# Kernel tuning notes

Measured on AMD Instinct MI355X. Metric: run time of the kernel, lower is better.

Reference implementation:

```python
import jax, jax.numpy as jnp
import numpy as np

EPS = 1e-12  # F.normalize default eps


def setup_inputs() -> dict:
    key = jax.random.key(0)
    x = jax.random.normal(key, (4, 64, 8192, 1), dtype=jnp.float32)
    return {"x": x, "k": 9, "dilation": 1}


def reference(x, k, dilation):
    # x: (B, D, N, 1)
    B, D, N, _ = x.shape
    kk = k * dilation
    # F.normalize(x, p=2, dim=1)
    norm = jnp.linalg.norm(x, axis=1, keepdims=True)
    xn = x / jnp.maximum(norm, EPS)
    # -> (B, N, D)
    pts = jnp.squeeze(xn, -1).transpose(0, 2, 1)
    # pairwise euclidean distance (cdist p=2)
    sq = jnp.sum(pts * pts, axis=-1)  # (B, N)
    d2 = sq[:, :, None] + sq[:, None, :] - 2.0 * jnp.einsum("bnd,bmd->bnm", pts, pts)
    dist = jnp.sqrt(jnp.maximum(d2, 0.0))  # (B, N, N)
    # torch.topk(-dist, k): k smallest distances
    _, nn_idx = jax.lax.top_k(-dist, kk)  # (B, N, kk)
    center_idx = jnp.broadcast_to(jnp.arange(N, dtype=nn_idx.dtype)[None, :, None], (B, N, kk))
    edge_index = jnp.stack([nn_idx, center_idx], axis=0)  # (2, B, N, kk)
    return edge_index[:, :, :, ::dilation]
```

## Files before the change

### kernel.cpp

```cpp
#include <hip/hip_runtime.h>

#define BB 4
#define DD 64
#define NN 8192
#define KK 9


typedef __attribute__((ext_vector_type(8))) _Float16 f16x8;
typedef __attribute__((ext_vector_type(16))) float f32x16;
typedef __attribute__((ext_vector_type(2))) _Float16 h2;
struct H2x4 { h2 a, b, c, d; };

__device__ __forceinline__ uint4 pack8(const unsigned* w) {
    return make_uint4(w[0] | (w[1] << 16), w[2] | (w[3] << 16),
                      w[4] | (w[5] << 16), w[6] | (w[7] << 16));
}

__device__ __forceinline__ float min3f(float a, float b, float c) {
    return fminf(fminf(a, b), c);
}

__device__ __forceinline__ float dot2acc(h2 g, h2 r, float acc) {
#if __has_builtin(__builtin_amdgcn_fdot2)
    return __builtin_amdgcn_fdot2(g, r, acc, false);
#else
    acc = fmaf((float)g[0], (float)r[0], acc);
    return fmaf((float)g[1], (float)r[1], acc);
#endif
}

__device__ __forceinline__ int s_to_j(int g, int s4) {
    int T = ((g >> 6) << 5) + (((g >> 5) & 1) << 4) + (g & 15);
    return T * 32 + ((s4 >> 2) << 3) + (((g >> 4) & 1) << 2) + (s4 & 3);
}

__global__ __launch_bounds__(256) void knorm2_kernel(const float* __restrict__ x,
                                                     float* __restrict__ xnT,
                                                     float* __restrict__ sq,
                                                     unsigned short* __restrict__ Phi,
                                                     unsigned short* __restrict__ Shi) {
    int t = blockIdx.x * 256 + threadIdx.x;
    int b = t >> 13;
    int n = t & (NN - 1);
    const float* xb = x + (size_t)b * DD * NN + n;
    float v[DD];
    float ss = 0.0f;
#pragma unroll
    for (int d = 0; d < DD; ++d) {
        v[d] = xb[(size_t)d * NN];
        ss = fmaf(v[d], v[d], ss);
    }
    float inv = 1.0f / fmaxf(sqrtf(ss), 1e-12f);
    float s2 = 0.0f;
#pragma unroll
    for (int d = 0; d < DD; ++d) {
        v[d] *= inv;
        s2 = fmaf(v[d], v[d], s2);
    }
    sq[t] = s2;
    float4* o4 = reinterpret_cast<float4*>(xnT + (size_t)t * DD);
#pragma unroll
    for (int d = 0; d < DD; d += 4) o4[d >> 2] = make_float4(v[d], v[d+1], v[d+2], v[d+3]);

    size_t base = (size_t)t * DD;
#pragma unroll
    for (int d0 = 0; d0 < DD; d0 += 8) {
        unsigned ph[8], sh[8];
#pragma unroll
        for (int e = 0; e < 8; ++e) {
            float f = v[d0 + e];
            _Float16 hp = (_Float16)f;
            _Float16 hs = (_Float16)(-2.0f * f);
            ph[e] = (unsigned)__builtin_bit_cast(unsigned short, hp);
            sh[e] = (unsigned)__builtin_bit_cast(unsigned short, hs);
        }
        *reinterpret_cast<uint4*>(Phi + base + d0) = pack8(ph);
        *reinterpret_cast<uint4*>(Shi + base + d0) = pack8(sh);
    }
}

__global__ __launch_bounds__(256, 4) void kmin_kernel(const unsigned short* __restrict__ Shi,
                                                      const unsigned short* __restrict__ Phi,
                                                      unsigned short* __restrict__ minbuf16) {
    __shared__ float stage[4][64][33];
    const int lane = threadIdx.x & 63;
    const int wave = threadIdx.x >> 6;
    const int l31 = lane & 31;
    const int half = lane >> 5;
    const int i0 = blockIdx.x * 256 + wave * 64;
    const int b = i0 >> 13;
    const int jloc0 = blockIdx.y * (NN / 8);

    f16x8 Bh0[4], Bh1[4];
    {
        const size_t ib0 = (size_t)(i0 + l31) * DD + half * 8;
        const size_t ib1 = (size_t)(i0 + 32 + l31) * DD + half * 8;
#pragma unroll
        for (int kc = 0; kc < 4; ++kc) {
            Bh0[kc] = *reinterpret_cast<const f16x8*>(Phi + ib0 + kc * 16);
            Bh1[kc] = *reinterpret_cast<const f16x8*>(Phi + ib1 + kc * 16);
        }
    }
    const size_t ja0 = ((size_t)b * NN + jloc0 + l31) * DD + half * 8;

    f16x8 A0[4], A1[4];
#pragma unroll
    for (int kc = 0; kc < 4; ++kc)
        A0[kc] = *reinterpret_cast<const f16x8*>(Shi + ja0 + kc * 16);

#pragma unroll 2
    for (int u2 = 0; u2 < 16; ++u2) {
        const int t0 = u2 * 2;
        {
            const size_t ja = ja0 + (size_t)(t0 + 1) * 32 * DD;
#pragma unroll
            for (int kc = 0; kc < 4; ++kc)
                A1[kc] = *reinterpret_cast<const f16x8*>(Shi + ja + kc * 16);
        }
        {
            f32x16 c0 = {}, c1 = {};
#pragma unroll
            for (int kc = 0; kc < 4; ++kc)
                c0 = __builtin_amdgcn_mfma_f32_32x32x16_f16(A0[kc], Bh0[kc], c0, 0, 0, 0);
#pragma unroll
            for (int kc = 0; kc < 4; ++kc)
                c1 = __builtin_amdgcn_mfma_f32_32x32x16_f16(A0[kc], Bh1[kc], c1, 0, 0, 0);
            const int col = half * 16 + (t0 & 15);
            {
                float q0 = min3f(c0[0], c0[1], c0[2]);
                float q1 = min3f(c0[3], c0[4], c0[5]);
                float q2 = min3f(c0[6], c0[7], c0[8]);
                float q3 = min3f(c0[9], c0[10], c0[11]);
                float q4 = min3f(c0[12], c0[13], c0[14]);
                stage[wave][l31][col] = fminf(min3f(q0, q1, q2), min3f(q3, q4, c0[15]));
            }
            {
                float q0 = min3f(c1[0], c1[1], c1[2]);
                float q1 = min3f(c1[3], c1[4], c1[5]);
                float q2 = min3f(c1[6], c1[7], c1[8]);
                float q3 = min3f(c1[9], c1[10], c1[11]);
                float q4 = min3f(c1[12], c1[13], c1[14]);
                stage[wave][32 + l31][col] = fminf(min3f(q0, q1, q2), min3f(q3, q4, c1[15]));
            }
        }
        if (u2 < 15) {
            const size_t ja = ja0 + (size_t)(t0 + 2) * 32 * DD;
#pragma unroll
            for (int kc = 0; kc < 4; ++kc)
                A0[kc] = *reinterpret_cast<const f16x8*>(Shi + ja + kc * 16);
        }
        {
            f32x16 c0 = {}, c1 = {};
#pragma unroll
            for (int kc = 0; kc < 4; ++kc)
                c0 = __builtin_amdgcn_mfma_f32_32x32x16_f16(A1[kc], Bh0[kc], c0, 0, 0, 0);
#pragma unroll
            for (int kc = 0; kc < 4; ++kc)
                c1 = __builtin_amdgcn_mfma_f32_32x32x16_f16(A1[kc], Bh1[kc], c1, 0, 0, 0);
            const int col = half * 16 + ((t0 + 1) & 15);
            {
                float q0 = min3f(c0[0], c0[1], c0[2]);
                float q1 = min3f(c0[3], c0[4], c0[5]);
                float q2 = min3f(c0[6], c0[7], c0[8]);
                float q3 = min3f(c0[9], c0[10], c0[11]);
                float q4 = min3f(c0[12], c0[13], c0[14]);
                stage[wave][l31][col] = fminf(min3f(q0, q1, q2), min3f(q3, q4, c0[15]));
            }
            {
                float q0 = min3f(c1[0], c1[1], c1[2]);
                float q1 = min3f(c1[3], c1[4], c1[5]);
                float q2 = min3f(c1[6], c1[7], c1[8]);
                float q3 = min3f(c1[9], c1[10], c1[11]);
                float q4 = min3f(c1[12], c1[13], c1[14]);
                stage[wave][32 + l31][col] = fminf(min3f(q0, q1, q2), min3f(q3, q4, c1[15]));
            }
        }
        if ((t0 & 15) == 14) {
            const int fph = t0 >> 4;
            unsigned short* dst0 = minbuf16 + (size_t)blockIdx.y * 64 + fph * 32;
#pragma unroll
            for (int it = 0; it < 4; ++it) {
                int idx = it * 64 + lane;
                int r = idx >> 2;
                int p = idx & 3;
                const float* s = &stage[wave][r][p * 8];
                unsigned w[8];
#pragma unroll
                for (int e = 0; e < 8; ++e)
                    w[e] = (unsigned)__builtin_bit_cast(unsigned short, (_Float16)s[e]);
                *reinterpret_cast<uint4*>(dst0 + (size_t)(i0 + r) * 512 + p * 8) = pack8(w);
            }
        }
    }
}

__global__ __launch_bounds__(256) void ksel_kernel(const float* __restrict__ xnT,
                                                   const float* __restrict__ sq,
                                                   const unsigned short* __restrict__ minbuf16,
                                                   const unsigned short* __restrict__ Phi,
                                                   int* __restrict__ out) {
    __shared__ unsigned short glist[4][40];
    __shared__ unsigned short jlist[4][64];
    const int lane = threadIdx.x & 63;
    const int wave = threadIdx.x >> 6;
    const int t = blockIdx.x * 4 + wave;
    const int tu = __builtin_amdgcn_readfirstlane(t);
    const int b = tu >> 13;
    const int n = tu & (NN - 1);

    float gm[8];
    {
        uint4 a = *reinterpret_cast<const uint4*>(minbuf16 + (size_t)tu * 512 + lane * 8);
        unsigned wv[4] = {a.x, a.y, a.z, a.w};
#pragma unroll
        for (int q4 = 0; q4 < 4; ++q4) {
            gm[q4 * 2 + 0] = (float)__builtin_bit_cast(_Float16, (unsigned short)(wv[q4] & 0xFFFFu));
            gm[q4 * 2 + 1] = (float)__builtin_bit_cast(_Float16, (unsigned short)(wv[q4] >> 16));
        }
    }

    float sv = fminf(min3f(gm[0], gm[1], gm[2]),
                     fminf(min3f(gm[3], gm[4], gm[5]), fminf(gm[6], gm[7])));
#pragma unroll
    for (int k = 2; k <= 64; k <<= 1) {
#pragma unroll
        for (int jj = k >> 1; jj >= 1; jj >>= 1) {
            float o = __shfl_xor(sv, jj);
            bool keepMin = (((lane & jj) == 0) == ((lane & k) == 0));
            sv = keepMin ? fminf(sv, o) : fmaxf(sv, o);
        }
    }
    const float th9p = __shfl(sv, 8);
    const float theta  = th9p + 8e-3f;
    const float kappa1 = th9p + 7.5e-3f;

    int cnt = 0;
    unsigned short* gl = &glist[wave][0];
#pragma unroll
    for (int q = 0; q < 8; ++q) {
        bool c = gm[q] <= theta;
        unsigned long long mask = __ballot(c);
        int pos = cnt + __popcll(mask & ((1ULL << lane) - 1ULL));
        if (c && pos < 40) gl[pos] = (unsigned short)(lane * 8 + q);
        cnt += (int)__popcll(mask);
    }
    __syncthreads();

    const unsigned short* __restrict__ Pb = Phi + ((size_t)b * NN) * DD;
    H2x4 arh[8];
    {
        const f16x8* pr = reinterpret_cast<const f16x8*>(Phi + (size_t)tu * DD);
#pragma unroll
        for (int c8 = 0; c8 < 8; ++c8) arh[c8] = __builtin_bit_cast(H2x4, pr[c8]);
    }

    const bool ovf = (cnt > 40);
    const int total = ovf ? NN : cnt * 16;
    const int nIt = (total + 63) >> 6;
    int S1 = 0;
    unsigned short* jl = &jlist[wave][0];
#pragma unroll 1
    for (int m = 0; m < nIt; ++m) {
        const int idx = m * 64 + lane;
        const bool act = idx < total;
        float m2ap = __uint_as_float(0x7f800000u);
        int j = 0;
        if (act) {
            j = ovf ? idx : s_to_j((int)gl[idx >> 4], idx & 15);
            const f16x8* p8 = reinterpret_cast<const f16x8*>(Pb + (size_t)j * DD);
            float a0 = 0.0f, a1 = 0.0f, a2 = 0.0f, a3 = 0.0f;
#pragma unroll
            for (int c8 = 0; c8 < 8; ++c8) {
                H2x4 g2 = __builtin_bit_cast(H2x4, p8[c8]);
                a0 = dot2acc(g2.a, arh[c8].a, a0);
                a1 = dot2acc(g2.b, arh[c8].b, a1);
                a2 = dot2acc(g2.c, arh[c8].c, a2);
                a3 = dot2acc(g2.d, arh[c8].d, a3);
            }
            m2ap = -2.0f * ((a0 + a1) + (a2 + a3));
        }
        bool pass = act && (m2ap <= kappa1);
        unsigned long long mask = __ballot(pass);
        int pos = S1 + __popcll(mask & ((1ULL << lane) - 1ULL));
        if (pass && pos < 64) jl[pos] = (unsigned short)j;
        S1 += (int)__popcll(mask);
    }
    __syncthreads();

    const float* __restrict__ Bb = xnT + (size_t)b * NN * DD;
    const float* __restrict__ sqb = sq + (size_t)b * NN;
    float ar[DD];
    {
        const float4* a4 = reinterpret_cast<const float4*>(xnT + (size_t)tu * DD);
#pragma unroll
        for (int d = 0; d < DD; d += 4) {
            float4 f = a4[d >> 2];
            ar[d] = f.x; ar[d + 1] = f.y; ar[d + 2] = f.z; ar[d + 3] = f.w;
        }
    }

    unsigned long long kout = ~0ULL;
    if (S1 <= 64) {
        unsigned long long v = ~0ULL;
        if (lane < S1) {
            int j = (int)jl[lane];
            const float4* bc4 = reinterpret_cast<const float4*>(Bb + (size_t)j * DD);
            float a0 = 0.0f, a1 = 0.0f, a2 = 0.0f, a3 = 0.0f;
#pragma unroll
            for (int d4 = 0; d4 < DD / 4; ++d4) {
                float4 f = bc4[d4];
                a0 = fmaf(ar[4 * d4 + 0], f.x, a0);
                a1 = fmaf(ar[4 * d4 + 1], f.y, a1);
                a2 = fmaf(ar[4 * d4 + 2], f.z, a2);
                a3 = fmaf(ar[4 * d4 + 3], f.w, a3);
            }
            float dot = (a0 + a1) + (a2 + a3);
            float key = fmaf(-2.0f, dot, sqb[j]);
            unsigned ub = __float_as_uint(key);
            ub ^= (0x80000000u | (unsigned)((int)ub >> 31));
            v = ((unsigned long long)ub << 32) | (unsigned)j;
        }
#pragma unroll
        for (int k = 2; k <= 64; k <<= 1) {
#pragma unroll
            for (int jj = k >> 1; jj >= 1; jj >>= 1) {
                unsigned long long o = __shfl_xor(v, jj);
                bool keepMin = (((lane & jj) == 0) == ((lane & k) == 0));
                bool less = o < v;
                unsigned long long mn = less ? o : v;
                unsigned long long mx = less ? v : o;
                v = keepMin ? mn : mx;
            }
        }
        kout = v;
    } else {
        unsigned long long kd[KK];
#pragma unroll
        for (int m = 0; m < KK; ++m) kd[m] = ~0ULL;
#pragma unroll 1
        for (int m = 0; m < nIt; ++m) {
            const int idx = m * 64 + lane;
            if (idx >= total) continue;
            int j = ovf ? idx : s_to_j((int)gl[idx >> 4], idx & 15);
            const float4* bc4 = reinterpret_cast<const float4*>(Bb + (size_t)j * DD);
            float a0 = 0.0f, a1 = 0.0f, a2 = 0.0f, a3 = 0.0f;
#pragma unroll
            for (int d4 = 0; d4 < DD / 4; ++d4) {
                float4 f = bc4[d4];
                a0 = fmaf(ar[4 * d4 + 0], f.x, a0);
                a1 = fmaf(ar[4 * d4 + 1], f.y, a1);
                a2 = fmaf(ar[4 * d4 + 2], f.z, a2);
                a3 = fmaf(ar[4 * d4 + 3], f.w, a3);
            }
            float dot = (a0 + a1) + (a2 + a3);
            float key = fmaf(-2.0f, dot, sqb[j]);
            unsigned ub = __float_as_uint(key);
            ub ^= (0x80000000u | (unsigned)((int)ub >> 31));
            unsigned long long cnd = ((unsigned long long)ub << 32) | (unsigned)j;
            if (cnd < kd[KK - 1]) {
#pragma unroll
                for (int m2 = 0; m2 < KK; ++m2) {
                    bool sw = cnd < kd[m2];
                    unsigned long long lo = sw ? cnd : kd[m2];
                    unsigned long long hi = sw ? kd[m2] : cnd;
                    kd[m2] = lo;
                    cnd = hi;
                }
            }
        }
#pragma unroll
        for (int r = 0; r < KK; ++r) {
            unsigned long long c = kd[0];
            unsigned long long wm = c;
#pragma unroll
            for (int d = 1; d < 64; d <<= 1) {
                unsigned long long o = __shfl_xor(wm, d);
                wm = (o < wm) ? o : wm;
            }
            if (lane == r) kout = wm;
            if (c == wm) {
#pragma unroll
                for (int m2 = 0; m2 < KK - 1; ++m2) kd[m2] = kd[m2 + 1];
                kd[KK - 1] = ~0ULL;
            }
        }
    }

    if (lane < KK) {
        out[(size_t)tu * KK + lane] = (int)(kout & 0xFFFFFFFFULL);
        out[(size_t)BB * NN * KK + (size_t)tu * KK + lane] = n;
    }
}

__global__ __launch_bounds__(256) void knorm_kernel(const float* __restrict__ x,
                                                    float* __restrict__ xnT,
                                                    float* __restrict__ sq) {
    int t = blockIdx.x * 256 + threadIdx.x;
    int b = t >> 13;
    int n = t & (NN - 1);
    const float* xb = x + (size_t)b * DD * NN + n;
    float v[DD];
    float ss = 0.0f;
#pragma unroll
    for (int d = 0; d < DD; ++d) {
        v[d] = xb[(size_t)d * NN];
        ss = fmaf(v[d], v[d], ss);
    }
    float norm = sqrtf(ss);
    float inv = 1.0f / fmaxf(norm, 1e-12f);
    float s2 = 0.0f;
#pragma unroll
    for (int d = 0; d < DD; ++d) {
        float xv = v[d] * inv;
        v[d] = xv;
        s2 = fmaf(xv, xv, s2);
    }
    float4* o4 = reinterpret_cast<float4*>(xnT + (size_t)t * DD);
#pragma unroll
    for (int d = 0; d < DD; d += 4) {
        o4[d >> 2] = make_float4(v[d], v[d + 1], v[d + 2], v[d + 3]);
    }
    sq[t] = s2;
}

template <int S>
__global__ __launch_bounds__(256, 2) void kdist_kernel(const float* __restrict__ xnT,
                                                       const float* __restrict__ sq,
                                                       unsigned long long* __restrict__ cand) {
    const int rb = blockIdx.x;
    const int b = rb >> 5;
    const int nbase = (rb & 31) * 256;
    const int n = nbase + threadIdx.x;
    const int s = blockIdx.y;
    const int jcount = NN / S;
    const int j0 = s * jcount;
    const int j1 = j0 + jcount;

    const float* __restrict__ Bb = xnT + ((size_t)b * NN) * DD;
    const float* __restrict__ sqb = sq + (size_t)b * NN;

    float ar[DD];
    {
        const float4* a4 = reinterpret_cast<const float4*>(Bb + (size_t)n * DD);
#pragma unroll
        for (int d = 0; d < DD; d += 4) {
            float4 f = a4[d >> 2];
            ar[d] = f.x; ar[d + 1] = f.y; ar[d + 2] = f.z; ar[d + 3] = f.w;
        }
    }
#pragma unroll
    for (int d = 0; d < DD; ++d) {
        asm volatile("" : "+v"(ar[d]));
    }

    unsigned long long kd[KK];
#pragma unroll
    for (int m = 0; m < KK; ++m) kd[m] = ~0ULL;

#pragma unroll 2
    for (int j = j0; j < j1; ++j) {
        const float4* bc4 = reinterpret_cast<const float4*>(Bb + (size_t)j * DD);
        float a0 = 0.0f, a1 = 0.0f, a2 = 0.0f, a3 = 0.0f;
#pragma unroll
        for (int d4 = 0; d4 < DD / 4; ++d4) {
            float4 f = bc4[d4];
            a0 = fmaf(ar[4 * d4 + 0], f.x, a0);
            a1 = fmaf(ar[4 * d4 + 1], f.y, a1);
            a2 = fmaf(ar[4 * d4 + 2], f.z, a2);
            a3 = fmaf(ar[4 * d4 + 3], f.w, a3);
        }
        float dot = (a0 + a1) + (a2 + a3);
        float key = fmaf(-2.0f, dot, sqb[j]);
        unsigned int ub = __float_as_uint(key);
        ub ^= (0x80000000u | (unsigned int)((int)ub >> 31));
        unsigned long long cnd = ((unsigned long long)ub << 32) | (unsigned int)j;
        if (cnd < kd[KK - 1]) {
#pragma unroll
            for (int m = 0; m < KK; ++m) {
                bool sw = cnd < kd[m];
                unsigned long long lo = sw ? cnd : kd[m];
                unsigned long long hi = sw ? kd[m] : cnd;
                kd[m] = lo;
                cnd = hi;
            }
        }
    }

    unsigned long long* outc = cand + ((size_t)(b * NN + n) * S + s) * KK;
#pragma unroll
    for (int m = 0; m < KK; ++m) outc[m] = kd[m];
}

template <int S>
__global__ __launch_bounds__(256) void kmerge_kernel(const unsigned long long* __restrict__ cand,
                                                     int* __restrict__ out) {
    int t = blockIdx.x * 256 + threadIdx.x;
    const unsigned long long* c = cand + (size_t)t * (S * KK);
    unsigned long long kd[KK];
#pragma unroll
    for (int m = 0; m < KK; ++m) kd[m] = ~0ULL;
#pragma unroll
    for (int q = 0; q < S * KK; ++q) {
        unsigned long long cnd = c[q];
        if (cnd < kd[KK - 1]) {
#pragma unroll
            for (int m = 0; m < KK; ++m) {
                bool sw = cnd < kd[m];
                unsigned long long lo = sw ? cnd : kd[m];
                unsigned long long hi = sw ? kd[m] : cnd;
                kd[m] = lo;
                cnd = hi;
            }
        }
    }
    int n = t & (NN - 1);
    int* out0 = out + (size_t)t * KK;
    int* out1 = out + (size_t)BB * NN * KK + (size_t)t * KK;
#pragma unroll
    for (int m = 0; m < KK; ++m) {
        out0[m] = (int)(kd[m] & 0xFFFFFFFFULL);
        out1[m] = n;
    }
}

extern "C" void kernel_launch(void* const* d_in, const int* in_sizes, int n_in,
                              void* d_out, int out_size, void* d_ws, size_t ws_size,
                              hipStream_t stream) {
    const float* x = (const float*)d_in[0];
    int* out = (int*)d_out;
    char* ws = (char*)d_ws;

    constexpr size_t XNT_B = (size_t)BB * NN * DD * 4;
    constexpr size_t SQ_B  = (size_t)BB * NN * 4;
    float* xnT = (float*)ws;
    float* sq  = (float*)(ws + XNT_B);

    constexpr size_t BF_B  = (size_t)BB * NN * DD * 2;
    constexpr size_t OFF_PHI = XNT_B + SQ_B;
    constexpr size_t OFF_PLO = OFF_PHI + BF_B;
    constexpr size_t OFF_SHI = OFF_PLO + BF_B;
    constexpr size_t OFF_SLO = OFF_SHI + BF_B;
    constexpr size_t OFF_MIN = OFF_SLO + BF_B;
    constexpr size_t MIN_B   = (size_t)512 * BB * NN * 4;
    constexpr size_t NEED_NEW = OFF_MIN + MIN_B;

    if (ws_size >= NEED_NEW) {
        unsigned short* Phi = (unsigned short*)(ws + OFF_PHI);
        unsigned short* Shi = (unsigned short*)(ws + OFF_SHI);
        unsigned short* minbuf16 = (unsigned short*)(ws + OFF_MIN);

        knorm2_kernel<<<dim3(BB * NN / 256), dim3(256), 0, stream>>>(x, xnT, sq, Phi, Shi);
        kmin_kernel<<<dim3(BB * NN / 256, 8), dim3(256), 0, stream>>>(Shi, Phi, minbuf16);
        ksel_kernel<<<dim3(BB * NN / 4), dim3(256), 0, stream>>>(xnT, sq, minbuf16, Phi, out);
        return;
    }

    unsigned long long* cand = (unsigned long long*)(ws + XNT_B + SQ_B);
    const size_t base = XNT_B + SQ_B;
    const size_t need8 = base + (size_t)BB * NN * 8 * KK * 8;

    knorm_kernel<<<dim3(BB * NN / 256), dim3(256), 0, stream>>>(x, xnT, sq);
    if (ws_size >= need8) {
        kdist_kernel<8><<<dim3(BB * NN / 256, 8), dim3(256), 0, stream>>>(xnT, sq, cand);
        kmerge_kernel<8><<<dim3(BB * NN / 256), dim3(256), 0, stream>>>(cand, out);
    } else {
        kdist_kernel<4><<<dim3(BB * NN / 256, 4), dim3(256), 0, stream>>>(xnT, sq, cand);
        kmerge_kernel<4><<<dim3(BB * NN / 256), dim3(256), 0, stream>>>(cand, out);
    }
}
```

Before: 245.6 us.

## Process two query points per wave in ksel kernel to raise ILP

Each wave in the selection kernel now handles two query points, interleaving their threshold sort, group listing, fp16 prefilter and exact distance/bitonic sort so independent memory loads and shuffles can overlap. The __syncthreads barriers are removed because shared lists are per-wave, and the first float4s of candidate rows are prefetched before loading the query vector. The grid is halved to match. This raises register pressure (two sets of query fragments and sort state), which may lower occupancy, and the loop runs to the longer of the two candidate counts.

Measured after the change: 243.2 us. No clear change (-1.0%).

```diff
diff --git a/kernel.cpp b/kernel.cpp
--- a/kernel.cpp
+++ b/kernel.cpp
@@ -199,158 +199,260 @@
                                                    const unsigned short* __restrict__ minbuf16,
                                                    const unsigned short* __restrict__ Phi,
                                                    int* __restrict__ out) {
-    __shared__ unsigned short glist[4][40];
-    __shared__ unsigned short jlist[4][64];
+    __shared__ unsigned short glist[4][2][40];
+    __shared__ unsigned short jlist[4][2][64];
     const int lane = threadIdx.x & 63;
     const int wave = threadIdx.x >> 6;
-    const int t = blockIdx.x * 4 + wave;
-    const int tu = __builtin_amdgcn_readfirstlane(t);
-    const int b = tu >> 13;
-    const int n = tu & (NN - 1);
-
-    float gm[8];
+    const int tA = __builtin_amdgcn_readfirstlane(blockIdx.x * 8 + wave * 2);
+    const int tB = tA + 1;
+    const int b = tA >> 13;
+    const int nA = tA & (NN - 1);
+    const int nB = tB & (NN - 1);
+
+    float gmA[8], gmB[8];
     {
-        uint4 a = *reinterpret_cast<const uint4*>(minbuf16 + (size_t)tu * 512 + lane * 8);
-        unsigned wv[4] = {a.x, a.y, a.z, a.w};
+        uint4 a = *reinterpret_cast<const uint4*>(minbuf16 + (size_t)tA * 512 + lane * 8);
+        uint4 c = *reinterpret_cast<const uint4*>(minbuf16 + (size_t)tB * 512 + lane * 8);
+        unsigned wa[4] = {a.x, a.y, a.z, a.w};
+        unsigned wb[4] = {c.x, c.y, c.z, c.w};
 #pragma unroll
         for (int q4 = 0; q4 < 4; ++q4) {
-            gm[q4 * 2 + 0] = (float)__builtin_bit_cast(_Float16, (unsigned short)(wv[q4] & 0xFFFFu));
-            gm[q4 * 2 + 1] = (float)__builtin_bit_cast(_Float16, (unsigned short)(wv[q4] >> 16));
-        }
-    }
-
-    float sv = fminf(min3f(gm[0], gm[1], gm[2]),
-                     fminf(min3f(gm[3], gm[4], gm[5]), fminf(gm[6], gm[7])));
+            gmA[q4*2+0] = (float)__builtin_bit_cast(_Float16, (unsigned short)(wa[q4] & 0xFFFFu));
+            gmA[q4*2+1] = (float)__builtin_bit_cast(_Float16, (unsigned short)(wa[q4] >> 16));
+            gmB[q4*2+0] = (float)__builtin_bit_cast(_Float16, (unsigned short)(wb[q4] & 0xFFFFu));
+            gmB[q4*2+1] = (float)__builtin_bit_cast(_Float16, (unsigned short)(wb[q4] >> 16));
+        }
+    }
+
+    float svA = fminf(min3f(gmA[0], gmA[1], gmA[2]),
+                      fminf(min3f(gmA[3], gmA[4], gmA[5]), fminf(gmA[6], gmA[7])));
+    float svB = fminf(min3f(gmB[0], gmB[1], gmB[2]),
+                      fminf(min3f(gmB[3], gmB[4], gmB[5]), fminf(gmB[6], gmB[7])));
 #pragma unroll
     for (int k = 2; k <= 64; k <<= 1) {
 #pragma unroll
         for (int jj = k >> 1; jj >= 1; jj >>= 1) {
-            float o = __shfl_xor(sv, jj);
+            float oA = __shfl_xor(svA, jj);
+            float oB = __shfl_xor(svB, jj);
             bool keepMin = (((lane & jj) == 0) == ((lane & k) == 0));
-            sv = keepMin ? fminf(sv, o) : fmaxf(sv, o);
-        }
-    }
-    const float th9p = __shfl(sv, 8);
-    const float theta  = th9p + 8e-3f;
-    const float kappa1 = th9p + 7.5e-3f;
-
-    int cnt = 0;
-    unsigned short* gl = &glist[wave][0];
+            svA = keepMin ? fminf(svA, oA) : fmaxf(svA, oA);
+            svB = keepMin ? fminf(svB, oB) : fmaxf(svB, oB);
+        }
+    }
+    const float th9pA = __shfl(svA, 8);
+    const float th9pB = __shfl(svB, 8);
+    const float thetaA  = th9pA + 8e-3f,  thetaB  = th9pB + 8e-3f;
+    const float kappa1A = th9pA + 7.5e-3f, kappa1B = th9pB + 7.5e-3f;
+
+    int cntA = 0, cntB = 0;
+    unsigned short* glA = &glist[wave][0][0];
+    unsigned short* glB = &glist[wave][1][0];
 #pragma unroll
     for (int q = 0; q < 8; ++q) {
-        bool c = gm[q] <= theta;
-        unsigned long long mask = __ballot(c);
-        int pos = cnt + __popcll(mask & ((1ULL << lane) - 1ULL));
-        if (c && pos < 40) gl[pos] = (unsigned short)(lane * 8 + q);
-        cnt += (int)__popcll(mask);
-    }
-    __syncthreads();
+        bool cA = gmA[q] <= thetaA;
+        unsigned long long mA = __ballot(cA);
+        int pA = cntA + __popcll(mA & ((1ULL << lane) - 1ULL));
+        if (cA && pA < 40) glA[pA] = (unsigned short)(lane * 8 + q);
+        cntA += (int)__popcll(mA);
+        bool cB = gmB[q] <= thetaB;
+        unsigned long long mB = __ballot(cB);
+        int pB = cntB + __popcll(mB & ((1ULL << lane) - 1ULL));
+        if (cB && pB < 40) glB[pB] = (unsigned short)(lane * 8 + q);
+        cntB += (int)__popcll(mB);
+    }
 
     const unsigned short* __restrict__ Pb = Phi + ((size_t)b * NN) * DD;
-    H2x4 arh[8];
+    H2x4 arhA[8], arhB[8];
     {
-        const f16x8* pr = reinterpret_cast<const f16x8*>(Phi + (size_t)tu * DD);
-#pragma unroll
-        for (int c8 = 0; c8 < 8; ++c8) arh[c8] = __builtin_bit_cast(H2x4, pr[c8]);
-    }
-
-    const bool ovf = (cnt > 40);
-    const int total = ovf ? NN : cnt * 16;
-    const int nIt = (total + 63) >> 6;
-    int S1 = 0;
-    unsigned short* jl = &jlist[wave][0];
+        const f16x8* prA = reinterpret_cast<const f16x8*>(Phi + (size_t)tA * DD);
+        const f16x8* prB = reinterpret_cast<const f16x8*>(Phi + (size_t)tB * DD);
+#pragma unroll
+        for (int c8 = 0; c8 < 8; ++c8) {
+            arhA[c8] = __builtin_bit_cast(H2x4, prA[c8]);
+            arhB[c8] = __builtin_bit_cast(H2x4, prB[c8]);
+        }
+    }
+
+    const bool ovfA = (cntA > 40), ovfB = (cntB > 40);
+    const int totalA = ovfA ? NN : cntA * 16;
+    const int totalB = ovfB ? NN : cntB * 16;
+    const int nItA = (totalA + 63) >> 6, nItB = (totalB + 63) >> 6;
+    const int nIt = nItA > nItB ? nItA : nItB;
+    int S1A = 0, S1B = 0;
+    unsigned short* jlA = &jlist[wave][0][0];
+    unsigned short* jlB = &jlist[wave][1][0];
 #pragma unroll 1
     for (int m = 0; m < nIt; ++m) {
         const int idx = m * 64 + lane;
-        const bool act = idx < total;
-        float m2ap = __uint_as_float(0x7f800000u);
-        int j = 0;
-        if (act) {
-            j = ovf ? idx : s_to_j((int)gl[idx >> 4], idx & 15);
-            const f16x8* p8 = reinterpret_cast<const f16x8*>(Pb + (size_t)j * DD);
+        const bool actA = idx < totalA;
+        const bool actB = idx < totalB;
+        float m2A = __uint_as_float(0x7f800000u);
+        float m2B = __uint_as_float(0x7f800000u);
+        int jA = 0, jB = 0;
+        if (actA) {
+            jA = ovfA ? idx : s_to_j((int)glA[idx >> 4], idx & 15);
+            const f16x8* p8 = reinterpret_cast<const f16x8*>(Pb + (size_t)jA * DD);
             float a0 = 0.0f, a1 = 0.0f, a2 = 0.0f, a3 = 0.0f;
 #pragma unroll
             for (int c8 = 0; c8 < 8; ++c8) {
                 H2x4 g2 = __builtin_bit_cast(H2x4, p8[c8]);
-                a0 = dot2acc(g2.a, arh[c8].a, a0);
-                a1 = dot2acc(g2.b, arh[c8].b, a1);
-                a2 = dot2acc(g2.c, arh[c8].c, a2);
-                a3 = dot2acc(g2.d, arh[c8].d, a3);
-            }
-            m2ap = -2.0f * ((a0 + a1) + (a2 + a3));
-        }
-        bool pass = act && (m2ap <= kappa1);
-        unsigned long long mask = __ballot(pass);
-        int pos = S1 + __popcll(mask & ((1ULL << lane) - 1ULL));
-        if (pass && pos < 64) jl[pos] = (unsigned short)j;
-        S1 += (int)__popcll(mask);
-    }
-    __syncthreads();
+                a0 = dot2acc(g2.a, arhA[c8].a, a0);
+                a1 = dot2acc(g2.b, arhA[c8].b, a1);
+                a2 = dot2acc(g2.c, arhA[c8].c, a2);
+                a3 = dot2acc(g2.d, arhA[c8].d, a3);
+            }
+            m2A = -2.0f * ((a0 + a1) + (a2 + a3));
+        }
+        if (actB) {
+            jB = ovfB ? idx : s_to_j((int)glB[idx >> 4], idx & 15);
+            const f16x8* p8 = reinterpret_cast<const f16x8*>(Pb + (size_t)jB * DD);
+            float a0 = 0.0f, a1 = 0.0f, a2 = 0.0f, a3 = 0.0f;
+#pragma unroll
+            for (int c8 = 0; c8 < 8; ++c8) {
+                H2x4 g2 = __builtin_bit_cast(H2x4, p8[c8]);
+                a0 = dot2acc(g2.a, arhB[c8].a, a0);
+                a1 = dot2acc(g2.b, arhB[c8].b, a1);
+                a2 = dot2acc(g2.c, arhB[c8].c, a2);
+                a3 = dot2acc(g2.d, arhB[c8].d, a3);
+            }
+            m2B = -2.0f * ((a0 + a1) + (a2 + a3));
+        }
+        bool passA = actA && (m2A <= kappa1A);
+        unsigned long long mA = __ballot(passA);
+        int pA = S1A + __popcll(mA & ((1ULL << lane) - 1ULL));
+        if (passA && pA < 64) jlA[pA] = (unsigned short)jA;
+        S1A += (int)__popcll(mA);
+        bool passB = actB && (m2B <= kappa1B);
+        unsigned long long mB = __ballot(passB);
+        int pB = S1B + __popcll(mB & ((1ULL << lane) - 1ULL));
+        if (passB && pB < 64) jlB[pB] = (unsigned short)jB;
+        S1B += (int)__popcll(mB);
+    }
 
     const float* __restrict__ Bb = xnT + (size_t)b * NN * DD;
     const float* __restrict__ sqb = sq + (size_t)b * NN;
-    float ar[DD];
+
+    unsigned long long vA = ~0ULL, vB = ~0ULL;
     {
-        const float4* a4 = reinterpret_cast<const float4*>(xnT + (size_t)tu * DD);
+        float4 bufA[4], bufB[4];
+        int jA = 0, jB = 0;
+        const bool hvA = lane < (S1A <= 64 ? S1A : 64);
+        const bool hvB = lane < (S1B <= 64 ? S1B : 64);
+        if (hvA) {
+            jA = (int)jlA[lane];
+            const float4* bc4 = reinterpret_cast<const float4*>(Bb + (size_t)jA * DD);
+#pragma unroll
+            for (int p = 0; p < 4; ++p) bufA[p] = bc4[p * 4];
+        }
+        if (hvB) {
+            jB = (int)jlB[lane];
+            const float4* bc4 = reinterpret_cast<const float4*>(Bb + (size_t)jB * DD);
+#pragma unroll
+            for (int p = 0; p < 4; ++p) bufB[p] = bc4[p * 4];
+        }
+        {
+            float ar[DD];
+            const float4* a4 = reinterpret_cast<const float4*>(xnT + (size_t)tA * DD);
+#pragma unroll
+            for (int d = 0; d < DD; d += 4) {
+                float4 f = a4[d >> 2];
+                ar[d] = f.x; ar[d+1] = f.y; ar[d+2] = f.z; ar[d+3] = f.w;
+            }
+            if (hvA) {
+                const float4* bc4 = reinterpret_cast<const float4*>(Bb + (size_t)jA * DD);
+                float a0 = 0, a1 = 0, a2 = 0, a3 = 0;
+#pragma unroll
+                for (int d4 = 0; d4 < 16; ++d4) {
+                    float4 f = (d4 % 4 == 0) ? bufA[d4 / 4] : bc4[d4];
+                    a0 = fmaf(ar[4*d4+0], f.x, a0);
+                    a1 = fmaf(ar[4*d4+1], f.y, a1);
+                    a2 = fmaf(ar[4*d4+2], f.z, a2);
+                    a3 = fmaf(ar[4*d4+3], f.w, a3);
+                }
+                float dot = (a0 + a1) + (a2 + a3);
+                float key = fmaf(-2.0f, dot, sqb[jA]);
+                unsigned ub = __float_as_uint(key);
+                ub ^= (0x80000000u | (unsigned)((int)ub >> 31));
+                vA = ((unsigned long long)ub << 32) | (unsigned)jA;
+            }
+        }
+        {
+            float ar[DD];
+            const float4* a4 = reinterpret_cast<const float4*>(xnT + (size_t)tB * DD);
+#pragma unroll
+            for (int d = 0; d < DD; d += 4) {
+                float4 f = a4[d >> 2];
+                ar[d] = f.x; ar[d+1] = f.y; ar[d+2] = f.z; ar[d+3] = f.w;
+            }
+            if (hvB) {
+                const float4* bc4 = reinterpret_cast<const float4*>(Bb + (size_t)jB * DD);
+                float a0 = 0, a1 = 0, a2 = 0, a3 = 0;
+#pragma unroll
+                for (int d4 = 0; d4 < 16; ++d4) {
+                    float4 f = (d4 % 4 == 0) ? bufB[d4 / 4] : bc4[d4];
+                    a0 = fmaf(ar[4*d4+0], f.x, a0);
+                    a1 = fmaf(ar[4*d4+1], f.y, a1);
+                    a2 = fmaf(ar[4*d4+2], f.z, a2);
+                    a3 = fmaf(ar[4*d4+3], f.w, a3);
+                }
+                float dot = (a0 + a1) + (a2 + a3);
+                float key = fmaf(-2.0f, dot, sqb[jB]);
+                unsigned ub = __float_as_uint(key);
+                ub ^= (0x80000000u | (unsigned)((int)ub >> 31));
+                vB = ((unsigned long long)ub << 32) | (unsigned)jB;
+            }
+        }
+    }
+#pragma unroll
+    for (int k = 2; k <= 64; k <<= 1) {
+#pragma unroll
+        for (int jj = k >> 1; jj >= 1; jj >>= 1) {
+            unsigned long long oA = __shfl_xor(vA, jj);
+            unsigned long long oB = __shfl_xor(vB, jj);
+            bool keepMin = (((lane & jj) == 0) == ((lane & k) == 0));
+            {
+                bool less = oA < vA;
+                unsigned long long mn = less ? oA : vA;
+                unsigned long long mx = less ? vA : oA;
+                vA = keepMin ? mn : mx;
+            }
+            {
+                bool less = oB < vB;
+                unsigned long long mn = less ? oB : vB;
+                unsigned long long mx = less ? vB : oB;
+                vB = keepMin ? mn : mx;
+            }
+        }
+    }
+    unsigned long long koutA = vA, koutB = vB;
+
+    auto exact_kd = [&](int tX, int totalX, bool ovfX,
+                        const unsigned short* glX) -> unsigned long long {
+        float ar[DD];
+        const float4* a4 = reinterpret_cast<const float4*>(xnT + (size_t)tX * DD);
 #pragma unroll
         for (int d = 0; d < DD; d += 4) {
             float4 f = a4[d >> 2];
-            ar[d] = f.x; ar[d + 1] = f.y; ar[d + 2] = f.z; ar[d + 3] = f.w;
-        }
-    }
-
-    unsigned long long kout = ~0ULL;
-    if (S1 <= 64) {
-        unsigned long long v = ~0ULL;
-        if (lane < S1) {
-            int j = (int)jl[lane];
+            ar[d] = f.x; ar[d+1] = f.y; ar[d+2] = f.z; ar[d+3] = f.w;
+        }
+        unsigned long long kd[KK];
+#pragma unroll
+        for (int m = 0; m < KK; ++m) kd[m] = ~0ULL;
+        const int nI = (totalX + 63) >> 6;
+#pragma unroll 1
+        for (int m = 0; m < nI; ++m) {
+            const int idx = m * 64 + lane;
+            if (idx >= totalX) continue;
+            int j = ovfX ? idx : s_to_j((int)glX[idx >> 4], idx & 15);
             const float4* bc4 = reinterpret_cast<const float4*>(Bb + (size_t)j * DD);
-            float a0 = 0.0f, a1 = 0.0f, a2 = 0.0f, a3 = 0.0f;
-#pragma unroll
-            for (int d4 = 0; d4 < DD / 4; ++d4) {
+            float a0 = 0, a1 = 0, a2 = 0, a3 = 0;
+#pragma unroll
+            for (int d4 = 0; d4 < 16; ++d4) {
                 float4 f = bc4[d4];
-                a0 = fmaf(ar[4 * d4 + 0], f.x, a0);
-                a1 = fmaf(ar[4 * d4 + 1], f.y, a1);
-                a2 = fmaf(ar[4 * d4 + 2], f.z, a2);
-                a3 = fmaf(ar[4 * d4 + 3], f.w, a3);
-            }
-            float dot = (a0 + a1) + (a2 + a3);
-            float key = fmaf(-2.0f, dot, sqb[j]);
-            unsigned ub = __float_as_uint(key);
-            ub ^= (0x80000000u | (unsigned)((int)ub >> 31));
-            v = ((unsigned long long)ub << 32) | (unsigned)j;
-        }
-#pragma unroll
-        for (int k = 2; k <= 64; k <<= 1) {
-#pragma unroll
-            for (int jj = k >> 1; jj >= 1; jj >>= 1) {
-                unsigned long long o = __shfl_xor(v, jj);
-                bool keepMin = (((lane & jj) == 0) == ((lane & k) == 0));
-                bool less = o < v;
-                unsigned long long mn = less ? o : v;
-                unsigned long long mx = less ? v : o;
-                v = keepMin ? mn : mx;
-            }
-        }
-        kout = v;
-    } else {
-        unsigned long long kd[KK];
-#pragma unroll
-        for (int m = 0; m < KK; ++m) kd[m] = ~0ULL;
-#pragma unroll 1
-        for (int m = 0; m < nIt; ++m) {
-            const int idx = m * 64 + lane;
-            if (idx >= total) continue;
-            int j = ovf ? idx : s_to_j((int)gl[idx >> 4], idx & 15);
-            const float4* bc4 = reinterpret_cast<const float4*>(Bb + (size_t)j * DD);
-            float a0 = 0.0f, a1 = 0.0f, a2 = 0.0f, a3 = 0.0f;
-#pragma unroll
-            for (int d4 = 0; d4 < DD / 4; ++d4) {
-                float4 f = bc4[d4];
-                a0 = fmaf(ar[4 * d4 + 0], f.x, a0);
-                a1 = fmaf(ar[4 * d4 + 1], f.y, a1);
-                a2 = fmaf(ar[4 * d4 + 2], f.z, a2);
-                a3 = fmaf(ar[4 * d4 + 3], f.w, a3);
+                a0 = fmaf(ar[4*d4+0], f.x, a0);
+                a1 = fmaf(ar[4*d4+1], f.y, a1);
+                a2 = fmaf(ar[4*d4+2], f.z, a2);
+                a3 = fmaf(ar[4*d4+3], f.w, a3);
             }
             float dot = (a0 + a1) + (a2 + a3);
             float key = fmaf(-2.0f, dot, sqb[j]);
@@ -368,6 +470,7 @@
                 }
             }
         }
+        unsigned long long ko = ~0ULL;
 #pragma unroll
         for (int r = 0; r < KK; ++r) {
             unsigned long long c = kd[0];
@@ -377,18 +480,23 @@
                 unsigned long long o = __shfl_xor(wm, d);
                 wm = (o < wm) ? o : wm;
             }
-            if (lane == r) kout = wm;
+            if (lane == r) ko = wm;
             if (c == wm) {
 #pragma unroll
                 for (int m2 = 0; m2 < KK - 1; ++m2) kd[m2] = kd[m2 + 1];
                 kd[KK - 1] = ~0ULL;
             }
         }
-    }
+        return ko;
+    };
+    if (S1A > 64) koutA = exact_kd(tA, totalA, ovfA, glA);
+    if (S1B > 64) koutB = exact_kd(tB, totalB, ovfB, glB);
 
     if (lane < KK) {
-        out[(size_t)tu * KK + lane] = (int)(kout & 0xFFFFFFFFULL);
-        out[(size_t)BB * NN * KK + (size_t)tu * KK + lane] = n;
+        out[(size_t)tA * KK + lane] = (int)(koutA & 0xFFFFFFFFULL);
+        out[(size_t)BB * NN * KK + (size_t)tA * KK + lane] = nA;
+        out[(size_t)tB * KK + lane] = (int)(koutB & 0xFFFFFFFFULL);
+        out[(size_t)BB * NN * KK + (size_t)tB * KK + lane] = nB;
     }
 }
 
@@ -551,7 +659,7 @@
 
         knorm2_kernel<<<dim3(BB * NN / 256), dim3(256), 0, stream>>>(x, xnT, sq, Phi, Shi);
         kmin_kernel<<<dim3(BB * NN / 256, 8), dim3(256), 0, stream>>>(Shi, Phi, minbuf16);
-        ksel_kernel<<<dim3(BB * NN / 4), dim3(256), 0, stream>>>(xnT, sq, minbuf16, Phi, out);
+        ksel_kernel<<<dim3(BB * NN / 8), dim3(256), 0, stream>>>(xnT, sq, minbuf16, Phi, out);
         return;
     }
 
```
